# Kernel optimization log

Hardware: AMD Instinct MI355X
Metric: run time of the kernel (lower is better)

## Reference

```python
import jax, jax.numpy as jnp
import numpy as np

N_USER, N_BIZ, E, D_IN, D_H, D_OUT = 100000, 50000, 500000, 256, 512, 256


def _sage(x_src, x_dst, src, dst, W_l, W_r, b):
    # SAGEConv with mean aggregation: lin_l(mean_{j in N(i)} x_src[j]) + lin_r(x_dst[i])
    n_dst = x_dst.shape[0]
    msg = x_src[src]                                             # [E, d_src]
    s = jax.ops.segment_sum(msg, dst, num_segments=n_dst)        # [n_dst, d_src]
    cnt = jax.ops.segment_sum(jnp.ones((dst.shape[0],), msg.dtype), dst,
                              num_segments=n_dst)                # [n_dst]
    mean = s / jnp.maximum(cnt, 1.0)[:, None]
    return mean @ W_l + b + x_dst @ W_r


def setup_inputs() -> dict:
    key = jax.random.key(0)
    ks = jax.random.split(key, 12)
    g = lambda k, shape: jax.random.normal(k, shape, jnp.float32) * (1.0 / np.sqrt(shape[0]))
    return {
        "x_user": jax.random.normal(ks[0], (N_USER, D_IN), jnp.float32),
        "x_biz": jax.random.normal(ks[1], (N_BIZ, D_IN), jnp.float32),
        "e_src": jax.random.randint(ks[2], (E,), 0, N_USER, jnp.int32),
        "e_dst": jax.random.randint(ks[3], (E,), 0, N_BIZ, jnp.int32),
        "W1_l_ub": g(ks[4], (D_IN, D_H)), "W1_r_ub": g(ks[5], (D_IN, D_H)),
        "b1_ub": jnp.zeros((D_H,), jnp.float32),
        "W1_l_bu": g(ks[6], (D_IN, D_H)), "W1_r_bu": g(ks[7], (D_IN, D_H)),
        "b1_bu": jnp.zeros((D_H,), jnp.float32),
        "W2_l_ub": g(ks[8], (D_H, D_OUT)), "W2_r_ub": g(ks[9], (D_H, D_OUT)),
        "b2_ub": jnp.zeros((D_OUT,), jnp.float32),
        "W2_l_bu": g(ks[10], (D_H, D_OUT)), "W2_r_bu": g(ks[11], (D_H, D_OUT)),
        "b2_bu": jnp.zeros((D_OUT,), jnp.float32),
    }


def reference(x_user, x_biz, e_src, e_dst,
              W1_l_ub, W1_r_ub, b1_ub, W1_l_bu, W1_r_bu, b1_bu,
              W2_l_ub, W2_r_ub, b2_ub, W2_l_bu, W2_r_bu, b2_bu):
    # Layer 1 (HeteroConv, aggr='sum'; each dst type has exactly one relation) + ReLU
    h_biz = jax.nn.relu(_sage(x_user, x_biz, e_src, e_dst, W1_l_ub, W1_r_ub, b1_ub))
    h_user = jax.nn.relu(_sage(x_biz, x_user, e_dst, e_src, W1_l_bu, W1_r_bu, b1_bu))
    # Layer 2 + ReLU
    o_biz = jax.nn.relu(_sage(h_user, h_biz, e_src, e_dst, W2_l_ub, W2_r_ub, b2_ub))
    o_user = jax.nn.relu(_sage(h_biz, h_user, e_dst, e_src, W2_l_bu, W2_r_bu, b2_bu))
    return o_user, o_biz
```

## Files before the change

### kernel.cpp

```cpp
#include <hip/hip_runtime.h>
#include <cstdint>
#include <cstddef>

typedef unsigned short u16;
typedef unsigned int u32;

typedef short bf16x8_t __attribute__((ext_vector_type(8)));
typedef float f32x4_t __attribute__((ext_vector_type(4)));

__device__ __forceinline__ u16 f2bf(float f) {
  u32 u = __float_as_uint(f);
  u += 0x7fffu + ((u >> 16) & 1u);
  return (u16)(u >> 16);
}
__device__ __forceinline__ float bf_lo(u32 w) { return __uint_as_float(w << 16); }
__device__ __forceinline__ float bf_hi(u32 w) { return __uint_as_float(w & 0xffff0000u); }
__device__ __forceinline__ u32 pack2(float lo, float hi) {
  return (u32)f2bf(lo) | ((u32)f2bf(hi) << 16);
}

__device__ __forceinline__ void glds16(const u16* g, u16* l) {
  __builtin_amdgcn_global_load_lds((const __attribute__((address_space(1))) void*)g,
                                   (__attribute__((address_space(3))) void*)l, 16, 0, 0);
}

__global__ __launch_bounds__(256) void cast_f32_to_bf16(
    const float* __restrict__ in, u16* __restrict__ out, int n4) {
  int i = blockIdx.x * 256 + threadIdx.x;
  if (i >= n4) return;
  float4 f = ((const float4*)in)[i];
  uint2 o;
  o.x = pack2(f.x, f.y);
  o.y = pack2(f.z, f.w);
  ((uint2*)out)[i] = o;
}

__global__ __launch_bounds__(256) void wt_cast(
    const float* __restrict__ W, u16* __restrict__ Wt, int K, int N) {
  int id = blockIdx.x * 256 + threadIdx.x;
  if (id >= K * N) return;
  int n_ = id / K;
  int k = id - n_ * K;
  Wt[id] = f2bf(W[(size_t)k * N + n_]);
}

__global__ __launch_bounds__(256) void zero_i32(int* __restrict__ p, int n) {
  int i = blockIdx.x * 256 + threadIdx.x;
  if (i < n) p[i] = 0;
}

__global__ __launch_bounds__(256) void count_kernel(
    const int* __restrict__ src, const int* __restrict__ dst,
    int* __restrict__ cb, int* __restrict__ cu, int E) {
  int e = blockIdx.x * 256 + threadIdx.x;
  if (e >= E) return;
  atomicAdd(&cb[dst[e]], 1);
  atomicAdd(&cu[src[e]], 1);
}

__device__ __forceinline__ void exscan_body(int* cnt, int* rp, int n) {
  __shared__ int buf[1024];
  const int tid = threadIdx.x;
  int chunk = (n + 1023) >> 10;
  int s = tid * chunk; if (s > n) s = n;
  int e = s + chunk; if (e > n) e = n;
  int sum = 0;
  for (int i = s; i < e; ++i) sum += cnt[i];
  buf[tid] = sum;
  __syncthreads();
  for (int off = 1; off < 1024; off <<= 1) {
    int t = (tid >= off) ? buf[tid - off] : 0;
    __syncthreads();
    buf[tid] += t;
    __syncthreads();
  }
  int run = (tid == 0) ? 0 : buf[tid - 1];
  for (int i = s; i < e; ++i) { int v = cnt[i]; rp[i] = run; cnt[i] = run; run += v; }
  if (tid == 0) rp[n] = buf[1023];
}

__global__ __launch_bounds__(1024) void exscan2_kernel(
    int* __restrict__ ca, int* __restrict__ rpa, int na,
    int* __restrict__ cb, int* __restrict__ rpb, int nb) {
  if (blockIdx.x == 0) exscan_body(ca, rpa, na);
  else exscan_body(cb, rpb, nb);
}

__global__ __launch_bounds__(256) void fill_kernel(
    const int* __restrict__ src, const int* __restrict__ dst,
    int* __restrict__ cb, int* __restrict__ cu,
    int* __restrict__ colb, int* __restrict__ colu, int E) {
  int e = blockIdx.x * 256 + threadIdx.x;
  if (e >= E) return;
  int s = src[e], d = dst[e];
  colb[atomicAdd(&cb[d], 1)] = s;
  colu[atomicAdd(&cu[s], 1)] = d;
}

__device__ __forceinline__ void acc4(float* a, uint2 p) {
  a[0] += bf_lo(p.x); a[1] += bf_hi(p.x);
  a[2] += bf_lo(p.y); a[3] += bf_hi(p.y);
}

__global__ __launch_bounds__(256) void agg_mean256(
    const u16* __restrict__ x, const int* __restrict__ rp,
    const int* __restrict__ col, u16* __restrict__ out, int M) {
  int wid = blockIdx.x * 4 + (threadIdx.x >> 6);
  if (wid >= M) return;
  int lane = threadIdx.x & 63;
  int s = rp[wid];
  int e = rp[wid + 1];
  float a[4] = {0.0f, 0.0f, 0.0f, 0.0f};
  const u16* xo = x + (size_t)lane * 4;
  int t = s;
  for (; t + 4 <= e; t += 4) {
    int j0 = col[t], j1 = col[t + 1], j2 = col[t + 2], j3 = col[t + 3];
    uint2 p0 = *(const uint2*)(xo + (size_t)j0 * 256);
    uint2 p1 = *(const uint2*)(xo + (size_t)j1 * 256);
    uint2 p2 = *(const uint2*)(xo + (size_t)j2 * 256);
    uint2 p3 = *(const uint2*)(xo + (size_t)j3 * 256);
    acc4(a, p0); acc4(a, p1); acc4(a, p2); acc4(a, p3);
  }
  for (; t < e; ++t) {
    uint2 p = *(const uint2*)(xo + (size_t)col[t] * 256);
    acc4(a, p);
  }
  int deg = e - s;
  float sc = 1.0f / (float)(deg > 0 ? deg : 1);
  uint2 o;
  o.x = pack2(a[0] * sc, a[1] * sc);
  o.y = pack2(a[2] * sc, a[3] * sc);
  *(uint2*)(out + (size_t)wid * 256 + (size_t)lane * 4) = o;
}

template <int NA, int HAS_C0, int RELU, int OUT_BF16, int HAS_BIAS>
__global__ __launch_bounds__(256) void gemm_kernel(
    const u16* __restrict__ A1, const u16* __restrict__ A2,
    const u16* __restrict__ B1t, const u16* __restrict__ B2t,
    const u16* __restrict__ C0, const float* __restrict__ bias,
    void* __restrict__ Cout, int M, int N, int K) {
  __shared__ u16 As[128 * 32];
  __shared__ u16 Bs[128 * 32];
  const int n0 = blockIdx.x * 128;
  const int m0 = blockIdx.y * 128;
  const int tid = threadIdx.x;
  const int w = tid >> 6;
  const int lane = tid & 63;
  const int wm = (w & 1) << 6;
  const int wn = (w >> 1) << 6;
  const int quad = lane >> 4;
  const int l16 = lane & 15;
  const int srow = (w << 5) + (lane >> 2);
  const int scol = (lane & 3) << 3;
  u16* lA = As + (w << 10);
  u16* lB = Bs + (w << 10);

  f32x4_t acc[4][4];
#pragma unroll
  for (int i = 0; i < 4; ++i)
#pragma unroll
    for (int j = 0; j < 4; ++j)
#pragma unroll
      for (int r = 0; r < 4; ++r) acc[i][j][r] = 0.0f;

#pragma unroll 1
  for (int pass = 0; pass < NA; ++pass) {
    const u16* A = pass ? A2 : A1;
    const u16* Bt = pass ? B2t : B1t;
#pragma unroll 1
    for (int k0 = 0; k0 < K; k0 += 32) {
      __syncthreads();
      const u16* gA = A + (size_t)(m0 + srow) * K + k0 + scol;
      const u16* gB = Bt + (size_t)(n0 + srow) * K + k0 + scol;
      glds16(gA, lA);
      glds16(gA + (size_t)16 * K, lA + 512);
      glds16(gB, lB);
      glds16(gB + (size_t)16 * K, lB + 512);
      __syncthreads();
      bf16x8_t af[4], bfv[4];
#pragma unroll
      for (int i = 0; i < 4; ++i)
        af[i] = *(const bf16x8_t*)(As + (wm + i * 16 + l16) * 32 + (quad << 3));
#pragma unroll
      for (int j = 0; j < 4; ++j)
        bfv[j] = *(const bf16x8_t*)(Bs + (wn + j * 16 + l16) * 32 + (quad << 3));
#pragma unroll
      for (int i = 0; i < 4; ++i)
#pragma unroll
        for (int j = 0; j < 4; ++j)
          acc[i][j] = __builtin_amdgcn_mfma_f32_16x16x32_bf16(af[i], bfv[j], acc[i][j], 0, 0, 0);
    }
  }

#pragma unroll
  for (int i = 0; i < 4; ++i) {
    int row = m0 + wm + i * 16 + (quad << 2);
#pragma unroll
    for (int j = 0; j < 4; ++j) {
      int colg = n0 + wn + j * 16 + l16;
      float b = HAS_BIAS ? bias[colg] : 0.0f;
#pragma unroll
      for (int r = 0; r < 4; ++r) {
        if (row + r < M) {
          float v = acc[i][j][r] + b;
          if (HAS_C0) v += bf_lo((u32)C0[(size_t)(row + r) * N + colg]);
          if (RELU) v = fmaxf(v, 0.0f);
          if (OUT_BF16)
            ((u16*)Cout)[(size_t)(row + r) * N + colg] = f2bf(v);
          else
            ((float*)Cout)[(size_t)(row + r) * N + colg] = v;
        }
      }
    }
  }
}

extern "C" void kernel_launch(void* const* d_in, const int* in_sizes, int n_in,
                              void* d_out, int out_size, void* d_ws, size_t ws_size,
                              hipStream_t stream) {
  const int DIN = 256, DH = 512, DOUT = 256;
  const int NU = in_sizes[0] / DIN;
  const int NB = in_sizes[1] / DIN;
  const int E = in_sizes[2];

  const float* x_user = (const float*)d_in[0];
  const float* x_biz = (const float*)d_in[1];
  const int* e_src = (const int*)d_in[2];
  const int* e_dst = (const int*)d_in[3];
  const float* W1l_ub = (const float*)d_in[4];
  const float* W1r_ub = (const float*)d_in[5];
  const float* b1_ub = (const float*)d_in[6];
  const float* W1l_bu = (const float*)d_in[7];
  const float* W1r_bu = (const float*)d_in[8];
  const float* b1_bu = (const float*)d_in[9];
  const float* W2l_ub = (const float*)d_in[10];
  const float* W2r_ub = (const float*)d_in[11];
  const float* b2_ub = (const float*)d_in[12];
  const float* W2l_bu = (const float*)d_in[13];
  const float* W2r_bu = (const float*)d_in[14];
  const float* b2_bu = (const float*)d_in[15];

  char* base = (char*)d_ws;
  size_t off = 0;
  auto alloc = [&](size_t bytes) -> char* {
    char* r = base + off;
    off += (bytes + 255) & ~(size_t)255;
    return r;
  };
  const size_t MARGIN = (size_t)128 * 512 * 2;

  int* rp_b = (int*)alloc((size_t)(NB + 1) * 4);
  int* rp_u = (int*)alloc((size_t)(NU + 1) * 4);
  int* cur_b = (int*)alloc((size_t)NB * 4);
  int* cur_u = (int*)alloc((size_t)NU * 4);
  int* col_b = (int*)alloc((size_t)E * 4);
  int* col_u = (int*)alloc((size_t)E * 4);
  u16* w1l_ub_t = (u16*)alloc((size_t)DIN * DH * 2);
  u16* w1r_ub_t = (u16*)alloc((size_t)DIN * DH * 2);
  u16* w1l_bu_t = (u16*)alloc((size_t)DIN * DH * 2);
  u16* w1r_bu_t = (u16*)alloc((size_t)DIN * DH * 2);
  u16* w2l_ub_t = (u16*)alloc((size_t)DH * DOUT * 2);
  u16* w2r_ub_t = (u16*)alloc((size_t)DH * DOUT * 2);
  u16* w2l_bu_t = (u16*)alloc((size_t)DH * DOUT * 2);
  u16* w2r_bu_t = (u16*)alloc((size_t)DH * DOUT * 2);
  u16* x_user_bf = (u16*)alloc((size_t)NU * DIN * 2 + MARGIN);
  u16* x_biz_bf = (u16*)alloc((size_t)NB * DIN * 2 + MARGIN);
  u16* m1_biz = (u16*)alloc((size_t)NB * DIN * 2 + MARGIN);
  u16* m1_user = (u16*)alloc((size_t)NU * DIN * 2 + MARGIN);
  u16* h_biz = (u16*)alloc((size_t)NB * DH * 2 + MARGIN);
  u16* h_user = (u16*)alloc((size_t)NU * DH * 2 + MARGIN);
  u16* t_user = x_user_bf;
  u16* t_biz = x_biz_bf;
  u16* m2t_biz = m1_biz;
  u16* m2t_user = m1_user;
  if (off > ws_size) return;

  {
    int n4u = NU * DIN / 4, n4b = NB * DIN / 4;
    cast_f32_to_bf16<<<(n4u + 255) / 256, 256, 0, stream>>>(x_user, x_user_bf, n4u);
    cast_f32_to_bf16<<<(n4b + 255) / 256, 256, 0, stream>>>(x_biz, x_biz_bf, n4b);
  }
  {
    int kn1 = DIN * DH, kn2 = DH * DOUT;
    wt_cast<<<(kn1 + 255) / 256, 256, 0, stream>>>(W1l_ub, w1l_ub_t, DIN, DH);
    wt_cast<<<(kn1 + 255) / 256, 256, 0, stream>>>(W1r_ub, w1r_ub_t, DIN, DH);
    wt_cast<<<(kn1 + 255) / 256, 256, 0, stream>>>(W1l_bu, w1l_bu_t, DIN, DH);
    wt_cast<<<(kn1 + 255) / 256, 256, 0, stream>>>(W1r_bu, w1r_bu_t, DIN, DH);
    wt_cast<<<(kn2 + 255) / 256, 256, 0, stream>>>(W2l_ub, w2l_ub_t, DH, DOUT);
    wt_cast<<<(kn2 + 255) / 256, 256, 0, stream>>>(W2r_ub, w2r_ub_t, DH, DOUT);
    wt_cast<<<(kn2 + 255) / 256, 256, 0, stream>>>(W2l_bu, w2l_bu_t, DH, DOUT);
    wt_cast<<<(kn2 + 255) / 256, 256, 0, stream>>>(W2r_bu, w2r_bu_t, DH, DOUT);
  }
  zero_i32<<<(NB + 255) / 256, 256, 0, stream>>>(cur_b, NB);
  zero_i32<<<(NU + 255) / 256, 256, 0, stream>>>(cur_u, NU);
  count_kernel<<<(E + 255) / 256, 256, 0, stream>>>(e_src, e_dst, cur_b, cur_u, E);
  exscan2_kernel<<<2, 1024, 0, stream>>>(cur_b, rp_b, NB, cur_u, rp_u, NU);
  fill_kernel<<<(E + 255) / 256, 256, 0, stream>>>(e_src, e_dst, cur_b, cur_u, col_b, col_u, E);
  agg_mean256<<<(NB + 3) / 4, 256, 0, stream>>>(x_user_bf, rp_b, col_b, m1_biz, NB);
  agg_mean256<<<(NU + 3) / 4, 256, 0, stream>>>(x_biz_bf, rp_u, col_u, m1_user, NU);
  {
    dim3 gb(DH / 128, (NB + 127) / 128);
    gemm_kernel<2, 0, 1, 1, 1><<<gb, 256, 0, stream>>>(
        m1_biz, x_biz_bf, w1l_ub_t, w1r_ub_t, nullptr, b1_ub, h_biz, NB, DH, DIN);
    dim3 gu(DH / 128, (NU + 127) / 128);
    gemm_kernel<2, 0, 1, 1, 1><<<gu, 256, 0, stream>>>(
        m1_user, x_user_bf, w1l_bu_t, w1r_bu_t, nullptr, b1_bu, h_user, NU, DH, DIN);
  }
  {
    dim3 gu(DOUT / 128, (NU + 127) / 128);
    gemm_kernel<1, 0, 0, 1, 0><<<gu, 256, 0, stream>>>(
        h_user, nullptr, w2l_ub_t, nullptr, nullptr, nullptr, t_user, NU, DOUT, DH);
    dim3 gb(DOUT / 128, (NB + 127) / 128);
    gemm_kernel<1, 0, 0, 1, 0><<<gb, 256, 0, stream>>>(
        h_biz, nullptr, w2l_bu_t, nullptr, nullptr, nullptr, t_biz, NB, DOUT, DH);
  }
  agg_mean256<<<(NB + 3) / 4, 256, 0, stream>>>(t_user, rp_b, col_b, m2t_biz, NB);
  agg_mean256<<<(NU + 3) / 4, 256, 0, stream>>>(t_biz, rp_u, col_u, m2t_user, NU);
  {
    float* o_user = (float*)d_out;
    float* o_biz = (float*)d_out + (size_t)NU * DOUT;
    dim3 gb(DOUT / 128, (NB + 127) / 128);
    gemm_kernel<1, 1, 1, 0, 1><<<gb, 256, 0, stream>>>(
        h_biz, nullptr, w2r_ub_t, nullptr, m2t_biz, b2_ub, o_biz, NB, DOUT, DH);
    dim3 gu(DOUT / 128, (NU + 127) / 128);
    gemm_kernel<1, 1, 1, 0, 1><<<gu, 256, 0, stream>>>(
        h_user, nullptr, w2r_bu_t, nullptr, m2t_user, b2_bu, o_user, NU, DOUT, DH);
  }
}
```

Measured before the change: 1.247 ms.

## Parallelize CSR prefix scan across tiles and merge paired aggregation launches

Replaces the two-block serial exclusive scan, where each thread walks a contiguous chunk sequentially, with a three-kernel tiled scan: per-tile sums, a small scan of the partials, then a wave-shuffle scan that writes the row pointers and cursors with vectorized int4 stores. It also merges the two mean-aggregation launches per layer into one launch that picks its graph direction from the block index. The goal is to remove the latency of the scan that used only two blocks and to cut launch overhead and tail idle time in aggregation. The new scan assumes at most 128 tiles and counts that are 16-byte aligned, which holds for these sizes.

```diff
diff --git a/kernel.cpp b/kernel.cpp
--- a/kernel.cpp
+++ b/kernel.cpp
@@ -58,32 +58,87 @@
   atomicAdd(&cu[src[e]], 1);
 }
 
-__device__ __forceinline__ void exscan_body(int* cnt, int* rp, int n) {
-  __shared__ int buf[1024];
-  const int tid = threadIdx.x;
-  int chunk = (n + 1023) >> 10;
-  int s = tid * chunk; if (s > n) s = n;
-  int e = s + chunk; if (e > n) e = n;
-  int sum = 0;
-  for (int i = s; i < e; ++i) sum += cnt[i];
-  buf[tid] = sum;
+__global__ __launch_bounds__(256) void tile_sums(
+    const int* __restrict__ c0, int* __restrict__ p0, int nt0, int n0,
+    const int* __restrict__ c1, int* __restrict__ p1, int nt1, int n1) {
+  const int* c = blockIdx.y ? c1 : c0;
+  int* p = blockIdx.y ? p1 : p0;
+  const int nt = blockIdx.y ? nt1 : nt0;
+  const int n = blockIdx.y ? n1 : n0;
+  if ((int)blockIdx.x >= nt) return;
+  int base = blockIdx.x * 1024 + threadIdx.x * 4;
+  int4 v = {0, 0, 0, 0};
+  if (base < n) v = *(const int4*)(c + base);
+  int s = v.x + v.y + v.z + v.w;
+  for (int off = 32; off; off >>= 1) s += __shfl_down(s, off, 64);
+  __shared__ int ws[4];
+  int lane = threadIdx.x & 63, w = threadIdx.x >> 6;
+  if (lane == 0) ws[w] = s;
   __syncthreads();
-  for (int off = 1; off < 1024; off <<= 1) {
+  if (threadIdx.x == 0) p[blockIdx.x] = ws[0] + ws[1] + ws[2] + ws[3];
+}
+
+__global__ __launch_bounds__(128) void scan_partials(
+    int* __restrict__ p0, int np0, int* __restrict__ rp0, int n0,
+    int* __restrict__ p1, int np1, int* __restrict__ rp1, int n1) {
+  int* p = blockIdx.x ? p1 : p0;
+  const int np = blockIdx.x ? np1 : np0;
+  int* rp = blockIdx.x ? rp1 : rp0;
+  const int n = blockIdx.x ? n1 : n0;
+  __shared__ int buf[128];
+  int tid = threadIdx.x;
+  int v = (tid < np) ? p[tid] : 0;
+  buf[tid] = v;
+  __syncthreads();
+  for (int off = 1; off < 128; off <<= 1) {
     int t = (tid >= off) ? buf[tid - off] : 0;
     __syncthreads();
     buf[tid] += t;
     __syncthreads();
   }
-  int run = (tid == 0) ? 0 : buf[tid - 1];
-  for (int i = s; i < e; ++i) { int v = cnt[i]; rp[i] = run; cnt[i] = run; run += v; }
-  if (tid == 0) rp[n] = buf[1023];
-}
-
-__global__ __launch_bounds__(1024) void exscan2_kernel(
-    int* __restrict__ ca, int* __restrict__ rpa, int na,
-    int* __restrict__ cb, int* __restrict__ rpb, int nb) {
-  if (blockIdx.x == 0) exscan_body(ca, rpa, na);
-  else exscan_body(cb, rpb, nb);
+  if (tid < np) p[tid] = buf[tid] - v;
+  if (tid == 0) rp[n] = buf[127];
+}
+
+__global__ __launch_bounds__(256) void scan_apply(
+    const int* __restrict__ c0, const int* __restrict__ p0,
+    int* __restrict__ rp0, int* __restrict__ cur0, int nt0, int n0,
+    const int* __restrict__ c1, const int* __restrict__ p1,
+    int* __restrict__ rp1, int* __restrict__ cur1, int nt1, int n1) {
+  const int* c = blockIdx.y ? c1 : c0;
+  const int* p = blockIdx.y ? p1 : p0;
+  int* rp = blockIdx.y ? rp1 : rp0;
+  int* cur = blockIdx.y ? cur1 : cur0;
+  const int nt = blockIdx.y ? nt1 : nt0;
+  const int n = blockIdx.y ? n1 : n0;
+  if ((int)blockIdx.x >= nt) return;
+  int base = blockIdx.x * 1024 + threadIdx.x * 4;
+  int4 v = {0, 0, 0, 0};
+  if (base < n) v = *(const int4*)(c + base);
+  int s = v.x + v.y + v.z + v.w;
+  int lane = threadIdx.x & 63, w = threadIdx.x >> 6;
+  int incl = s;
+  for (int off = 1; off < 64; off <<= 1) {
+    int t = __shfl_up(incl, off, 64);
+    if (lane >= off) incl += t;
+  }
+  __shared__ int ws[4];
+  if (lane == 63) ws[w] = incl;
+  __syncthreads();
+  int woff = 0;
+#pragma unroll
+  for (int q = 0; q < 4; ++q)
+    if (q < w) woff += ws[q];
+  int excl = incl - s + woff + p[blockIdx.x];
+  if (base < n) {
+    int4 r;
+    r.x = excl;
+    r.y = excl + v.x;
+    r.z = r.y + v.y;
+    r.w = r.z + v.z;
+    *(int4*)(rp + base) = r;
+    *(int4*)(cur + base) = r;
+  }
 }
 
 __global__ __launch_bounds__(256) void fill_kernel(
@@ -102,10 +157,22 @@
   a[2] += bf_lo(p.y); a[3] += bf_hi(p.y);
 }
 
-__global__ __launch_bounds__(256) void agg_mean256(
-    const u16* __restrict__ x, const int* __restrict__ rp,
-    const int* __restrict__ col, u16* __restrict__ out, int M) {
-  int wid = blockIdx.x * 4 + (threadIdx.x >> 6);
+__global__ __launch_bounds__(256) void agg_mean256_dual(
+    const u16* __restrict__ xa, const int* __restrict__ rpa,
+    const int* __restrict__ cola, u16* __restrict__ outa, int Ma,
+    const u16* __restrict__ xb, const int* __restrict__ rpb,
+    const int* __restrict__ colb, u16* __restrict__ outb, int Mb) {
+  const int nblk_a = (Ma + 3) >> 2;
+  const u16* x;
+  const int *rp, *col;
+  u16* out;
+  int M, wid0;
+  if ((int)blockIdx.x < nblk_a) {
+    x = xa; rp = rpa; col = cola; out = outa; M = Ma; wid0 = blockIdx.x * 4;
+  } else {
+    x = xb; rp = rpb; col = colb; out = outb; M = Mb; wid0 = (blockIdx.x - nblk_a) * 4;
+  }
+  int wid = wid0 + (threadIdx.x >> 6);
   if (wid >= M) return;
   int lane = threadIdx.x & 63;
   int s = rp[wid];
@@ -253,6 +320,8 @@
   int* rp_u = (int*)alloc((size_t)(NU + 1) * 4);
   int* cur_b = (int*)alloc((size_t)NB * 4);
   int* cur_u = (int*)alloc((size_t)NU * 4);
+  int* part_b = (int*)alloc(128 * 4);
+  int* part_u = (int*)alloc(128 * 4);
   int* col_b = (int*)alloc((size_t)E * 4);
   int* col_u = (int*)alloc((size_t)E * 4);
   u16* w1l_ub_t = (u16*)alloc((size_t)DIN * DH * 2);
@@ -275,6 +344,9 @@
   u16* m2t_user = m1_user;
   if (off > ws_size) return;
 
+  const int nt_b = (NB + 1023) / 1024;
+  const int nt_u = (NU + 1023) / 1024;
+
   {
     int n4u = NU * DIN / 4, n4b = NB * DIN / 4;
     cast_f32_to_bf16<<<(n4u + 255) / 256, 256, 0, stream>>>(x_user, x_user_bf, n4u);
@@ -294,10 +366,18 @@
   zero_i32<<<(NB + 255) / 256, 256, 0, stream>>>(cur_b, NB);
   zero_i32<<<(NU + 255) / 256, 256, 0, stream>>>(cur_u, NU);
   count_kernel<<<(E + 255) / 256, 256, 0, stream>>>(e_src, e_dst, cur_b, cur_u, E);
-  exscan2_kernel<<<2, 1024, 0, stream>>>(cur_b, rp_b, NB, cur_u, rp_u, NU);
+  tile_sums<<<dim3(nt_u, 2), 256, 0, stream>>>(cur_b, part_b, nt_b, NB,
+                                               cur_u, part_u, nt_u, NU);
+  scan_partials<<<2, 128, 0, stream>>>(part_b, nt_b, rp_b, NB,
+                                       part_u, nt_u, rp_u, NU);
+  scan_apply<<<dim3(nt_u, 2), 256, 0, stream>>>(cur_b, part_b, rp_b, cur_b, nt_b, NB,
+                                                cur_u, part_u, rp_u, cur_u, nt_u, NU);
   fill_kernel<<<(E + 255) / 256, 256, 0, stream>>>(e_src, e_dst, cur_b, cur_u, col_b, col_u, E);
-  agg_mean256<<<(NB + 3) / 4, 256, 0, stream>>>(x_user_bf, rp_b, col_b, m1_biz, NB);
-  agg_mean256<<<(NU + 3) / 4, 256, 0, stream>>>(x_biz_bf, rp_u, col_u, m1_user, NU);
+  {
+    int nblk = (NB + 3) / 4 + (NU + 3) / 4;
+    agg_mean256_dual<<<nblk, 256, 0, stream>>>(x_user_bf, rp_b, col_b, m1_biz, NB,
+                                               x_biz_bf, rp_u, col_u, m1_user, NU);
+  }
   {
     dim3 gb(DH / 128, (NB + 127) / 128);
     gemm_kernel<2, 0, 1, 1, 1><<<gb, 256, 0, stream>>>(
@@ -314,8 +394,11 @@
     gemm_kernel<1, 0, 0, 1, 0><<<gb, 256, 0, stream>>>(
         h_biz, nullptr, w2l_bu_t, nullptr, nullptr, nullptr, t_biz, NB, DOUT, DH);
   }
-  agg_mean256<<<(NB + 3) / 4, 256, 0, stream>>>(t_user, rp_b, col_b, m2t_biz, NB);
-  agg_mean256<<<(NU + 3) / 4, 256, 0, stream>>>(t_biz, rp_u, col_u, m2t_user, NU);
+  {
+    int nblk = (NB + 3) / 4 + (NU + 3) / 4;
+    agg_mean256_dual<<<nblk, 256, 0, stream>>>(t_user, rp_b, col_b, m2t_biz, NB,
+                                               t_biz, rp_u, col_u, m2t_user, NU);
+  }
   {
     float* o_user = (float*)d_out;
     float* o_biz = (float*)d_out + (size_t)NU * DOUT;
```

Result: faster. 1.024 ms (-17.9%).
